# Kernel optimization log

Hardware: AMD Instinct MI355X
Metric: run time of the kernel (lower is better)

The kernel has to match this reference:

```python
import jax, jax.numpy as jnp
import numpy as np

B, S, D = 1024, 192, 512
MAX_ITEMS, NUM_LAYERS = 64, 3
LN_EPS = 1e-5


def setup_inputs() -> dict:
    key = jax.random.key(0)
    k_tok, k_pad, k_item, k_layer, k_temp = jax.random.split(key, 5)
    token_embeddings = jax.random.normal(k_tok, (B, S, D), dtype=jnp.float32)
    # Left-padded mask: zeros then contiguous ones until the end of the row.
    pad_len = jax.random.randint(k_pad, (B,), 0, S)  # at least 1 real token
    attention_mask = (jnp.arange(S)[None, :] >= pad_len[:, None]).astype(jnp.int32)
    item_pos_emb = 0.01 * jax.random.normal(k_item, (MAX_ITEMS, D), dtype=jnp.float32)
    layer_emb = 0.01 * jax.random.normal(k_layer, (NUM_LAYERS, D), dtype=jnp.float32)
    temporal_decay = 0.02 * jax.random.normal(k_temp, (MAX_ITEMS, D), dtype=jnp.float32)
    ln_weight = jnp.ones((D,), dtype=jnp.float32)
    ln_bias = jnp.zeros((D,), dtype=jnp.float32)
    return {
        "token_embeddings": token_embeddings,
        "attention_mask": attention_mask,
        "item_pos_emb": item_pos_emb,
        "layer_emb": layer_emb,
        "temporal_decay": temporal_decay,
        "ln_weight": ln_weight,
        "ln_bias": ln_bias,
    }


def reference(token_embeddings, attention_mask, item_pos_emb, layer_emb,
              temporal_decay, ln_weight, ln_bias):
    mask = attention_mask > 0                              # (B, S) bool
    has_content = jnp.any(mask, axis=1)                    # (B,)
    start = jnp.argmax(mask, axis=1)                       # first non-pad index
    end = S - jnp.argmax(mask[:, ::-1], axis=1)            # last non-pad index + 1
    idx = jnp.arange(S)[None, :]                           # (1, S)
    pos = idx - start[:, None]                             # content-relative position
    in_range = (pos >= 0) & (idx < end[:, None]) & has_content[:, None]
    pos_c = jnp.clip(pos, 0)
    item_idx = jnp.where(in_range, pos_c // NUM_LAYERS, 0)  # (B, S)
    layer_idx = jnp.where(in_range, pos_c % NUM_LAYERS, 0)
    add = item_pos_emb[item_idx] + layer_emb[layer_idx] + temporal_decay[item_idx]
    enhanced = token_embeddings + jnp.where(in_range[..., None], add, 0.0)
    # LayerNorm over last dim
    mu = jnp.mean(enhanced, axis=-1, keepdims=True)
    var = jnp.mean(jnp.square(enhanced - mu), axis=-1, keepdims=True)
    normed = (enhanced - mu) * jax.lax.rsqrt(var + LN_EPS) * ln_weight + ln_bias
    # zero out padding (dropout is identity in eval mode)
    return normed * attention_mask[..., None].astype(normed.dtype)
```

## Files before the change

kernel.cpp:

```cpp
#include <hip/hip_runtime.h>

typedef float f4 __attribute__((ext_vector_type(4)));

#define BB 1024
#define SS 192
#define DD 512
#define NUM_LAYERS 3
#define LN_EPS 1e-5f
#define ZERO_BLOCKS 512
#define CONT_BLOCKS 2048
#define MAIN_BLOCKS (ZERO_BLOCKS + CONT_BLOCKS)
#define CONT_WAVES (CONT_BLOCKS * 4)

__global__ __launch_bounds__(256) void prep_kernel(
    const int* __restrict__ mask,
    const float* __restrict__ item_pos,
    const float* __restrict__ layer_emb,
    const float* __restrict__ decay,
    float* __restrict__ add_tab,
    int* __restrict__ start)
{
    const int tid = threadIdx.x;
    if (blockIdx.x < SS) {
        const int p = blockIdx.x;
        if (tid < DD / 4) {
            const int item = p / NUM_LAYERS;
            const int layer = p - item * NUM_LAYERS;
            const f4 iv = reinterpret_cast<const f4*>(item_pos + item * DD)[tid];
            const f4 lv = reinterpret_cast<const f4*>(layer_emb + layer * DD)[tid];
            const f4 dv = reinterpret_cast<const f4*>(decay + item * DD)[tid];
            reinterpret_cast<f4*>(add_tab + p * DD)[tid] = iv + lv + dv;
        }
        return;
    }
    const int b = (blockIdx.x - SS) * 4 + (tid >> 6);
    const int lane = tid & 63;
    if (b < BB) {
        const int* m = mask + b * SS;
        const unsigned long long b0 = __ballot(m[lane] > 0);
        const unsigned long long b1 = __ballot(m[lane + 64] > 0);
        const unsigned long long b2 = __ballot(m[lane + 128] > 0);
        int idx;
        if (b0)      idx = __ffsll(b0) - 1;
        else if (b1) idx = 64 + __ffsll(b1) - 1;
        else if (b2) idx = 128 + __ffsll(b2) - 1;
        else         idx = SS;
        if (lane == 0) start[b] = idx;
    }
}

__global__ __launch_bounds__(1024) void scan_kernel(
    const int* __restrict__ start, int* __restrict__ P, int* __restrict__ nc)
{
    __shared__ int sh[1024];
    const int t = threadIdx.x;
    const int cnt = SS - start[t];
    sh[t] = cnt;
    __syncthreads();
    #pragma unroll
    for (int off = 1; off < 1024; off <<= 1) {
        const int u = (t >= off) ? sh[t - off] : 0;
        __syncthreads();
        sh[t] += u;
        __syncthreads();
    }
    P[t] = sh[t] - cnt;
    if (t == 1023) { P[1024] = sh[1023]; *nc = sh[1023]; }
}

template <int CTRL>
__device__ __forceinline__ float dpp_x(float v) {
    return __uint_as_float((unsigned)__builtin_amdgcn_update_dpp(
            0, (int)__float_as_uint(v), CTRL, 0xF, 0xF, true));
}
__device__ __forceinline__ float swz16(float v) {
    return __uint_as_float((unsigned)__builtin_amdgcn_ds_swizzle(
            (int)__float_as_uint(v), 0x401f));
}
__device__ __forceinline__ float bper32(float v, int xaddr32) {
    return __uint_as_float((unsigned)__builtin_amdgcn_ds_bpermute(
            xaddr32, (int)__float_as_uint(v)));
}

__device__ __forceinline__ void wave_allreduce2(float& v0, float& v1, int xaddr32) {
    v0 += dpp_x<0xB1>(v0);  v1 += dpp_x<0xB1>(v1);
    v0 += dpp_x<0x4E>(v0);  v1 += dpp_x<0x4E>(v1);
    v0 += dpp_x<0x141>(v0); v1 += dpp_x<0x141>(v1);
    v0 += dpp_x<0x140>(v0); v1 += dpp_x<0x140>(v1);
    v0 += swz16(v0);        v1 += swz16(v1);
    v0 += bper32(v0, xaddr32); v1 += bper32(v1, xaddr32);
}

__global__ __launch_bounds__(256) void main_kernel(
    const float* __restrict__ tok,
    const float* __restrict__ add_tab,
    const float* __restrict__ lnw,
    const float* __restrict__ lnb,
    const int* __restrict__ start,
    const int* __restrict__ P,
    const int* __restrict__ nc,
    float* __restrict__ out)
{
    const int tid = threadIdx.x;

    if (blockIdx.x < ZERO_BLOCKS) {
        const f4 z = {0.f, 0.f, 0.f, 0.f};
        #pragma unroll
        for (int q = 0; q < 2; ++q) {
            const int b = blockIdx.x * 2 + q;
            const int st = start[b];
            f4* o4 = reinterpret_cast<f4*>(out + (size_t)b * SS * DD);
            const int nf4 = st * (DD / 4);
            for (int i = tid; i < nf4; i += 256)
                o4[i] = z;
        }
        return;
    }

    const int wid = tid >> 6;
    const int lane = tid & 63;
    const int l0 = lane;
    const int l1 = lane + 64;
    const int xaddr32 = (lane ^ 32) << 2;

    const f4 w0 = reinterpret_cast<const f4*>(lnw)[l0];
    const f4 w1 = reinterpret_cast<const f4*>(lnw)[l1];
    const f4 c0 = reinterpret_cast<const f4*>(lnb)[l0];
    const f4 c1 = reinterpret_cast<const f4*>(lnb)[l1];

    const int wave = (blockIdx.x - ZERO_BLOCKS) * 4 + wid;
    const int Nc = *nc;
    const int nq = (Nc + CONT_WAVES - 1) / CONT_WAVES;
    const int gs = wave * nq;
    if (gs >= Nc) return;
    const int ge = (gs + nq < Nc) ? gs + nq : Nc;

    int lo = 0, hi = BB;
    while (lo < hi) {
        const int mid = (lo + hi + 1) >> 1;
        if (P[mid] <= gs) lo = mid; else hi = mid - 1;
    }
    int b = lo;
    int pb = P[b], pb1 = P[b + 1];

    #pragma unroll 1
    for (int g = gs; g < ge; ++g) {
        if (g >= pb1) {
            do { ++b; pb1 = P[b + 1]; } while (g >= pb1);
            pb = P[b];
        }
        const int pos = g - pb;
        const int st = SS - (pb1 - pb);
        const int row = b * SS + st + pos;

        const f4* x4 = reinterpret_cast<const f4*>(tok + (size_t)row * DD);
        const f4 xv0 = x4[l0];
        const f4 xv1 = x4[l1];

        const f4* a4 = reinterpret_cast<const f4*>(add_tab + pos * DD);
        const f4 y0 = xv0 + a4[l0];
        const f4 y1 = xv1 + a4[l1];

        float sum = (y0.x + y0.y) + (y0.z + y0.w)
                  + (y1.x + y1.y) + (y1.z + y1.w);
        const f4 q0 = y0 * y0;
        const f4 q1 = y1 * y1;
        float sq = (q0.x + q0.y) + (q0.z + q0.w)
                 + (q1.x + q1.y) + (q1.z + q1.w);

        wave_allreduce2(sum, sq, xaddr32);

        const float mu  = sum * (1.0f / DD);
        const float var = sq * (1.0f / DD) - mu * mu;
        const float inv = rsqrtf(var + LN_EPS);

        f4* o4 = reinterpret_cast<f4*>(out + (size_t)row * DD);
        o4[l0] = (y0 - mu) * inv * w0 + c0;
        o4[l1] = (y1 - mu) * inv * w1 + c1;
    }
}

extern "C" void kernel_launch(void* const* d_in, const int* in_sizes, int n_in,
                              void* d_out, int out_size, void* d_ws, size_t ws_size,
                              hipStream_t stream) {
    const float* tok       = (const float*)d_in[0];
    const int*   mask      = (const int*)d_in[1];
    const float* item_pos  = (const float*)d_in[2];
    const float* layer_emb = (const float*)d_in[3];
    const float* decay     = (const float*)d_in[4];
    const float* lnw       = (const float*)d_in[5];
    const float* lnb       = (const float*)d_in[6];
    float* out = (float*)d_out;

    int*   nc      = (int*)d_ws;
    float* add_tab = (float*)((char*)d_ws + 256);
    int*   start   = (int*)((char*)add_tab + (size_t)SS * DD * sizeof(float));
    int*   P       = (int*)((char*)start + BB * sizeof(int));

    prep_kernel<<<SS + 256, 256, 0, stream>>>(mask, item_pos, layer_emb, decay,
                                              add_tab, start);
    scan_kernel<<<1, 1024, 0, stream>>>(start, P, nc);
    main_kernel<<<MAIN_BLOCKS, 256, 0, stream>>>(tok, add_tab, lnw, lnb,
                                                 start, P, nc, out);
}
```

Measured before the change: 144.1 us.

## Balance padding zero-fill across all blocks using a prefix scan of pad sizes

Adds a second prefix scan over per-row padding sizes. Every main-kernel block now clears an equal slice of the padded output before doing its share of content rows, replacing the 512 dedicated zero blocks that each handled two rows of uneven padding length. The goal is to remove load imbalance in the zero-fill and to overlap the zero stores with LayerNorm work in the same blocks. In exchange the single-block scan kernel does twice the work, and each block runs an extra binary search.

```diff
diff --git a/kernel.cpp b/kernel.cpp
--- a/kernel.cpp
+++ b/kernel.cpp
@@ -7,10 +7,9 @@
 #define DD 512
 #define NUM_LAYERS 3
 #define LN_EPS 1e-5f
-#define ZERO_BLOCKS 512
-#define CONT_BLOCKS 2048
-#define MAIN_BLOCKS (ZERO_BLOCKS + CONT_BLOCKS)
-#define CONT_WAVES (CONT_BLOCKS * 4)
+#define NBLK 2048
+#define NWAVES (NBLK * 4)
+#define RPB (SS * (DD / 4))
 
 __global__ __launch_bounds__(256) void prep_kernel(
     const int* __restrict__ mask,
@@ -50,11 +49,14 @@
 }
 
 __global__ __launch_bounds__(1024) void scan_kernel(
-    const int* __restrict__ start, int* __restrict__ P, int* __restrict__ nc)
+    const int* __restrict__ start,
+    int* __restrict__ P, int* __restrict__ Z, int* __restrict__ tot)
 {
     __shared__ int sh[1024];
     const int t = threadIdx.x;
-    const int cnt = SS - start[t];
+    const int st = start[t];
+
+    const int cnt = SS - st;
     sh[t] = cnt;
     __syncthreads();
     #pragma unroll
@@ -65,7 +67,21 @@
         __syncthreads();
     }
     P[t] = sh[t] - cnt;
-    if (t == 1023) { P[1024] = sh[1023]; *nc = sh[1023]; }
+    if (t == 1023) { P[1024] = sh[1023]; tot[0] = sh[1023]; }
+    __syncthreads();
+
+    const int zc = st * (DD / 4);
+    sh[t] = zc;
+    __syncthreads();
+    #pragma unroll
+    for (int off = 1; off < 1024; off <<= 1) {
+        const int u = (t >= off) ? sh[t - off] : 0;
+        __syncthreads();
+        sh[t] += u;
+        __syncthreads();
+    }
+    Z[t] = sh[t] - zc;
+    if (t == 1023) { Z[1024] = sh[1023]; tot[1] = sh[1023]; }
 }
 
 template <int CTRL>
@@ -96,25 +112,39 @@
     const float* __restrict__ add_tab,
     const float* __restrict__ lnw,
     const float* __restrict__ lnb,
-    const int* __restrict__ start,
     const int* __restrict__ P,
-    const int* __restrict__ nc,
+    const int* __restrict__ Z,
+    const int* __restrict__ tot,
     float* __restrict__ out)
 {
     const int tid = threadIdx.x;
 
-    if (blockIdx.x < ZERO_BLOCKS) {
-        const f4 z = {0.f, 0.f, 0.f, 0.f};
-        #pragma unroll
-        for (int q = 0; q < 2; ++q) {
-            const int b = blockIdx.x * 2 + q;
-            const int st = start[b];
-            f4* o4 = reinterpret_cast<f4*>(out + (size_t)b * SS * DD);
-            const int nf4 = st * (DD / 4);
-            for (int i = tid; i < nf4; i += 256)
-                o4[i] = z;
+    {
+        const int ZT = tot[1];
+        const int zq = (ZT + NBLK - 1) / NBLK;
+        int g = blockIdx.x * zq;
+        const int ze0 = g + zq;
+        const int ze = ze0 < ZT ? ze0 : ZT;
+        if (g < ze) {
+            int lo = 0, hi = BB;
+            while (lo < hi) {
+                const int mid = (lo + hi + 1) >> 1;
+                if (Z[mid] <= g) lo = mid; else hi = mid - 1;
+            }
+            int b = lo;
+            const f4 zv = {0.f, 0.f, 0.f, 0.f};
+            while (g < ze) {
+                int zb1 = Z[b + 1];
+                while (g >= zb1) { ++b; zb1 = Z[b + 1]; }
+                const int zb = Z[b];
+                const int lim = ze < zb1 ? ze : zb1;
+                f4* dst = reinterpret_cast<f4*>(out) + (size_t)b * RPB + (g - zb);
+                const int n = lim - g;
+                for (int i = tid; i < n; i += 256)
+                    dst[i] = zv;
+                g = lim;
+            }
         }
-        return;
     }
 
     const int wid = tid >> 6;
@@ -128,9 +158,9 @@
     const f4 c0 = reinterpret_cast<const f4*>(lnb)[l0];
     const f4 c1 = reinterpret_cast<const f4*>(lnb)[l1];
 
-    const int wave = (blockIdx.x - ZERO_BLOCKS) * 4 + wid;
-    const int Nc = *nc;
-    const int nq = (Nc + CONT_WAVES - 1) / CONT_WAVES;
+    const int wave = blockIdx.x * 4 + wid;
+    const int Nc = tot[0];
+    const int nq = (Nc + NWAVES - 1) / NWAVES;
     const int gs = wave * nq;
     if (gs >= Nc) return;
     const int ge = (gs + nq < Nc) ? gs + nq : Nc;
@@ -192,14 +222,14 @@
     const float* lnb       = (const float*)d_in[6];
     float* out = (float*)d_out;
 
-    int*   nc      = (int*)d_ws;
+    int*   tot     = (int*)d_ws;
     float* add_tab = (float*)((char*)d_ws + 256);
     int*   start   = (int*)((char*)add_tab + (size_t)SS * DD * sizeof(float));
-    int*   P       = (int*)((char*)start + BB * sizeof(int));
+    int*   P       = start + BB;
+    int*   Z       = P + BB + 1;
 
     prep_kernel<<<SS + 256, 256, 0, stream>>>(mask, item_pos, layer_emb, decay,
                                               add_tab, start);
-    scan_kernel<<<1, 1024, 0, stream>>>(start, P, nc);
-    main_kernel<<<MAIN_BLOCKS, 256, 0, stream>>>(tok, add_tab, lnw, lnb,
-                                                 start, P, nc, out);
-}
+    scan_kernel<<<1, 1024, 0, stream>>>(start, P, Z, tot);
+    main_kernel<<<NBLK, 256, 0, stream>>>(tok, add_tab, lnw, lnb, P, Z, tot, out);
+}
```

Result: slower. 148.0 us (+2.7%).
